# Optimization experiments

Measured on AMD Instinct MI355X. Metric: run time of the kernel, lower is better.

The kernel has to match this reference:

```python
import jax, jax.numpy as jnp
import numpy as np

B, M, N = 2, 256, 256
K, P, Q, D = 8, 512, 512, 64
R, Pp, Qp, Dp = 128, 512, 512, 64
TEMP = float(np.sqrt(Dp))  # softmax temperature = sqrt(D')


def _xavier(key, shape):
    # xavier_uniform over last two dims (fan_in, fan_out), matching torch init on (K, d, D)
    fan_in, fan_out = shape[-2], shape[-1]
    lim = float(np.sqrt(6.0 / (fan_in + fan_out)))
    return jax.random.uniform(key, shape, jnp.float32, -lim, lim)


def setup_inputs() -> dict:
    key = jax.random.key(0)
    ks = jax.random.split(key, 9)
    return {
        "z": jax.random.normal(ks[0], (B, M, N, R), jnp.float32),
        "y_q": jax.random.normal(ks[1], (B, N, Qp), jnp.float32),
        "x_k": jax.random.normal(ks[2], (B, M, Pp), jnp.float32),
        "Theta_x": _xavier(ks[3], (K, P, D)),
        "Theta_y": _xavier(ks[4], (K, Q, D)),
        "Lam_x": _xavier(ks[5], (K, Pp, Dp)),
        "Lam_y": _xavier(ks[6], (K, Qp, Dp)),
        "Lam_zx": _xavier(ks[7], (K, R, Dp)),
        "Lam_zy": _xavier(ks[8], (K, R, Dp)),
    }


def reference(z, y_q, x_k, Theta_x, Theta_y, Lam_x, Lam_y, Lam_zx, Lam_zy):
    # --- mixed attention scores ---
    xt = jnp.einsum('bmp,kpd->bkmd', x_k, Lam_x)          # [B,K,M,D']
    yt = jnp.einsum('bnq,kqd->bknd', y_q, Lam_y)          # [B,K,N,D']
    r = jnp.einsum('bkmd,bknd->bkmn', xt, yt)             # pairwise term
    zy = jnp.einsum('bmnr,krd->bkmnd', z, Lam_zy)         # [B,K,M,N,D'] (large)
    r = r + jnp.einsum('bkmnd,bkmd->bkmn', zy, xt)
    r = r + jnp.einsum('bknd,bmnr,krd->bkmn', yt, z, Lam_zx)
    # --- generalised convolution (mask=None, bias=False) ---
    a = jax.nn.softmax(r / TEMP, axis=-2)                 # softmax over M (column-wise)
    xv = jnp.einsum('bmp,kpd->bkmd', x_k, Theta_x)        # value projection
    y = jnp.einsum('bkmn,bkmd,kqd->bnq', a, xv, Theta_y)  # [B,N,Q]
    return y
```

## Files before the change

kernel.cpp:

```cpp
#include <hip/hip_runtime.h>
#include <hip/hip_bf16.h>

#define LOG2E_OVER_T 0.18033688011112042f

typedef __attribute__((ext_vector_type(8))) short short8;
typedef __attribute__((ext_vector_type(4))) float f32x4;
typedef unsigned short ushort_t;
typedef unsigned long long ull_t;

#define MFMA16(a, b, c) __builtin_amdgcn_mfma_f32_16x16x32_bf16(a, b, c, 0, 0, 0)

__device__ __forceinline__ ushort_t f2bf(float f) {
    union { float f; unsigned u; } v; v.f = f;
    unsigned r = (v.u + 0x7fffu + ((v.u >> 16) & 1u)) >> 16;
    return (ushort_t)r;
}

__device__ __forceinline__ void gload16(const float* g, float* l) {
    __builtin_amdgcn_global_load_lds(
        (const __attribute__((address_space(1))) void*)g,
        (__attribute__((address_space(3))) void*)l, 16, 0, 0);
}

__device__ __forceinline__ void split8(const float4 a, const float4 b,
                                       short8& hi, short8& lo)
{
    union { float f[8]; unsigned u[8]; } Z;
    Z.f[0] = a.x; Z.f[1] = a.y; Z.f[2] = a.z; Z.f[3] = a.w;
    Z.f[4] = b.x; Z.f[5] = b.y; Z.f[6] = b.z; Z.f[7] = b.w;
    union { unsigned u[4]; short8 s; } H, L;
    #pragma unroll
    for (int i = 0; i < 4; i++) {
        const unsigned u0 = Z.u[2 * i], u1 = Z.u[2 * i + 1];
        H.u[i] = __builtin_amdgcn_perm(u1, u0, 0x07060302u);
        union { unsigned u; float f; } h0, h1;
        h0.u = u0 & 0xffff0000u; h1.u = u1 & 0xffff0000u;
        union { float f; unsigned u; } l0, l1;
        l0.f = Z.f[2 * i] - h0.f; l1.f = Z.f[2 * i + 1] - h1.f;
        L.u[i] = __builtin_amdgcn_perm(l1.u, l0.u, 0x07060302u);
    }
    hi = H.s; lo = L.s;
}

__device__ __forceinline__ void mfma_core64(
    const ushort_t* __restrict__ Ag, int lda,
    const ushort_t* __restrict__ Btg, int ldb,
    int ksteps, f32x4 acc[2][2])
{
    __shared__ __align__(16) ushort_t As[64 * 40];
    __shared__ __align__(16) ushort_t Bs[64 * 40];
    const int t = threadIdx.x;
    const int srow = t >> 2, skc = (t & 3) * 8;
    const int lane = t & 63, w = t >> 6;
    const int wr = w >> 1, wc = w & 1;
    const int fr = lane & 15, kg = lane >> 4;
    const int aoff = (wr * 32 + fr) * 40 + kg * 8;
    const int boff = (wc * 32 + fr) * 40 + kg * 8;
    const long arow = (long)srow * lda + skc;
    const long brow = (long)srow * ldb + skc;

    short8 ra = *(const short8*)(Ag + arow);
    short8 rb = *(const short8*)(Btg + brow);
    for (int kt = 0; kt < ksteps; kt++) {
        __syncthreads();
        *(short8*)&As[srow * 40 + skc] = ra;
        *(short8*)&Bs[srow * 40 + skc] = rb;
        __syncthreads();
        if (kt + 1 < ksteps) {
            ra = *(const short8*)(Ag + arow + (kt + 1) * 32);
            rb = *(const short8*)(Btg + brow + (kt + 1) * 32);
        }
        short8 a0 = *(const short8*)&As[aoff];
        short8 a1 = *(const short8*)&As[aoff + 16 * 40];
        short8 b0 = *(const short8*)&Bs[boff];
        short8 b1 = *(const short8*)&Bs[boff + 16 * 40];
        acc[0][0] = MFMA16(a0, b0, acc[0][0]);
        acc[0][1] = MFMA16(a0, b1, acc[0][1]);
        acc[1][0] = MFMA16(a1, b0, acc[1][0]);
        acc[1][1] = MFMA16(a1, b1, acc[1][1]);
    }
}

__device__ __forceinline__ void zero_acc(f32x4 acc[2][2]) {
    const f32x4 z4 = {0.f, 0.f, 0.f, 0.f};
    acc[0][0] = z4; acc[0][1] = z4; acc[1][0] = z4; acc[1][1] = z4;
}

__global__ __launch_bounds__(256)
void convert_kernel(const float* __restrict__ x_k, const float* __restrict__ y_q,
                    const float* __restrict__ Lam_x, const float* __restrict__ Theta_x,
                    const float* __restrict__ Lam_y, const float* __restrict__ Lam_zy,
                    const float* __restrict__ Lam_zx, const float* __restrict__ Theta_y,
                    ushort_t* __restrict__ xkb, ushort_t* __restrict__ yqb,
                    ushort_t* __restrict__ WxTb, ushort_t* __restrict__ WyTb,
                    ushort_t* __restrict__ Zyb, ushort_t* __restrict__ Zxb,
                    ushort_t* __restrict__ TyTb, float* __restrict__ ssum)
{
    int i = blockIdx.x * 256 + threadIdx.x;
    if (i < 262144) { xkb[i] = f2bf(x_k[i]); return; }
    i -= 262144;
    if (i < 262144) { yqb[i] = f2bf(y_q[i]); return; }
    i -= 262144;
    if (i < 524288) {
        const int k = i >> 16, rem = i & 65535, dc = rem >> 9, p = i & 511;
        const float v = (dc < 64) ? Lam_x[((long)k * 512 + p) * 64 + dc]
                                  : Theta_x[((long)k * 512 + p) * 64 + dc - 64];
        WxTb[i] = f2bf(v); return;
    }
    i -= 524288;
    if (i < 262144) {
        const int k = i >> 15, d = (i >> 9) & 63, p = i & 511;
        WyTb[i] = f2bf(Lam_y[((long)k * 512 + p) * 64 + d]); return;
    }
    i -= 262144;
    if (i < 65536) { Zyb[i] = f2bf(Lam_zy[i]); return; }
    i -= 65536;
    if (i < 65536) { Zxb[i] = f2bf(Lam_zx[i]); return; }
    i -= 65536;
    if (i < 262144) {
        const int q = i >> 9, kd = i & 511, k = kd >> 6, d = kd & 63;
        TyTb[i] = f2bf(Theta_y[((long)k * 512 + q) * 64 + d]); return;
    }
    i -= 262144;
    ssum[i] = 0.f;
}

__global__ __launch_bounds__(256)
void proj_kernel(const ushort_t* __restrict__ xkb, const ushort_t* __restrict__ yqb,
                 const ushort_t* __restrict__ WxTb, const ushort_t* __restrict__ WyTb,
                 ushort_t* __restrict__ xtb, ushort_t* __restrict__ ytb,
                 ushort_t* __restrict__ xvTb)
{
    const int side = blockIdx.z;
    const int bx = blockIdx.x, by = blockIdx.y;
    if (side == 1 && bx >= 8) return;
    f32x4 acc[2][2]; zero_acc(acc);
    const int t = threadIdx.x, lane = t & 63, w = t >> 6;
    const int wr = w >> 1, wc = w & 1, fr = lane & 15, kg = lane >> 4;

    if (side == 0) {
        mfma_core64(xkb + (long)(by * 64) * 512, 512,
                    WxTb + (long)(bx * 64) * 512, 512, 16, acc);
        const int k = bx >> 1, isxv = bx & 1;
        #pragma unroll
        for (int mi = 0; mi < 2; mi++)
        #pragma unroll
        for (int ni = 0; ni < 2; ni++) {
            const int grow0 = by * 64 + wr * 32 + mi * 16 + kg * 4;
            const int b = grow0 >> 8, m0 = grow0 & 255;
            const int d = wc * 32 + ni * 16 + fr;
            if (!isxv) {
                #pragma unroll
                for (int j = 0; j < 4; j++)
                    xtb[(((long)(b * 8 + k)) * 256 + m0 + j) * 64 + d] = f2bf(acc[mi][ni][j]);
            } else {
                ull_t pk = (ull_t)f2bf(acc[mi][ni][0])
                         | ((ull_t)f2bf(acc[mi][ni][1]) << 16)
                         | ((ull_t)f2bf(acc[mi][ni][2]) << 32)
                         | ((ull_t)f2bf(acc[mi][ni][3]) << 48);
                *(ull_t*)&xvTb[(((long)(b * 8 + k)) * 64 + d) * 256 + m0] = pk;
            }
        }
    } else {
        mfma_core64(yqb + (long)(by * 64) * 512, 512,
                    WyTb + (long)(bx * 64) * 512, 512, 16, acc);
        const int k = bx;
        #pragma unroll
        for (int mi = 0; mi < 2; mi++)
        #pragma unroll
        for (int ni = 0; ni < 2; ni++)
        #pragma unroll
        for (int j = 0; j < 4; j++) {
            const int grow = by * 64 + wr * 32 + mi * 16 + kg * 4 + j;
            const int b = grow >> 8, n = grow & 255;
            const int d = wc * 32 + ni * 16 + fr;
            ytb[(((long)(b * 8 + k)) * 256 + n) * 64 + d] = f2bf(acc[mi][ni][j]);
        }
    }
}

__global__ __launch_bounds__(256)
void step2_kernel(const ushort_t* __restrict__ xtb, const ushort_t* __restrict__ ytb,
                  const ushort_t* __restrict__ Zyb, const ushort_t* __restrict__ Zxb,
                  ushort_t* __restrict__ wzyb, ushort_t* __restrict__ wzxb,
                  float* __restrict__ t1)
{
    const int bz = blockIdx.x;
    const int t = threadIdx.x, lane = t & 63, w = t >> 6;
    const int wr = w >> 1, wc = w & 1, fr = lane & 15, kg = lane >> 4;

    if (bz < 256) {
        const int which = bz >> 7, idx = bz & 127;
        const int bk = idx >> 3, tile = idx & 7, mt = tile >> 1, nt = tile & 1;
        const int k = bk & 7, b = bk >> 3;
        const ushort_t* Ag  = (which ? ytb : xtb) + ((long)bk * 256 + mt * 64) * 64;
        const ushort_t* Btg = (which ? Zxb : Zyb) + ((long)k * 128 + nt * 64) * 64;
        ushort_t* C = which ? wzxb : wzyb;
        f32x4 acc[2][2]; zero_acc(acc);
        mfma_core64(Ag, 64, Btg, 64, 2, acc);
        #pragma unroll
        for (int mi = 0; mi < 2; mi++)
        #pragma unroll
        for (int ni = 0; ni < 2; ni++)
        #pragma unroll
        for (int j = 0; j < 4; j++) {
            const int m_glob = mt * 64 + wr * 32 + mi * 16 + kg * 4 + j;
            const int r_glob = nt * 64 + wc * 32 + ni * 16 + fr;
            C[(((long)b * 256 + m_glob) * 8 + k) * 128 + r_glob] = f2bf(acc[mi][ni][j]);
        }
    } else {
        const int idx = bz - 256;
        const int bk = idx >> 4, tile = idx & 15, nt2 = tile >> 2, mt2 = tile & 3;
        f32x4 acc[2][2]; zero_acc(acc);
        mfma_core64(ytb + ((long)bk * 256 + nt2 * 64) * 64, 64,
                    xtb + ((long)bk * 256 + mt2 * 64) * 64, 64, 2, acc);
        #pragma unroll
        for (int mi = 0; mi < 2; mi++)
        #pragma unroll
        for (int ni = 0; ni < 2; ni++)
        #pragma unroll
        for (int j = 0; j < 4; j++) {
            const int n_glob = nt2 * 64 + wr * 32 + mi * 16 + kg * 4 + j;
            const int m_glob = mt2 * 64 + wc * 32 + ni * 16 + fr;
            t1[((long)bk * 256 + n_glob) * 256 + m_glob] = acc[mi][ni][j];
        }
    }
}

__global__ __launch_bounds__(256)
void fused_score(const float* __restrict__ z,
                 const ushort_t* __restrict__ wzyb, const ushort_t* __restrict__ wzxb,
                 const float* __restrict__ t1, ushort_t* __restrict__ Et,
                 float* __restrict__ ssum)
{
    const int nt = blockIdx.x, mt = blockIdx.y, b = blockIdx.z;
    const int nbase = nt * 16, m0 = mt * 8;
    __shared__ __align__(16) float zs[8192];
    __shared__ float sc[4][8][8][17];

    const int tid = threadIdx.x;
    const int lane = tid & 63, w = tid >> 6;
    const int fr = lane & 15, kg = lane >> 4;
    const int f8 = fr & 7;

    const int js   = w * 512 + lane;
    for (int c = 0; c < 2; c++) {
        const int n0c = nbase + c * 8;

        #pragma unroll
        for (int i = 0; i < 8; i++) {
            const int j   = js + i * 64;
            const int row = j >> 5;
            const int m_l = row >> 3, n_l = row & 7;
            const int sl  = (j & 31) ^ ((m_l ^ n_l) & 7);
            const float* src = z + (((long)b * 256 + m0 + m_l) * 256 + n0c + n_l) * 128 + sl * 4;
            gload16(src, &zs[(w * 8 + i) * 256]);
        }
        __syncthreads();

        #pragma unroll
        for (int m = 0; m < 8; m++) {
            const int row = m * 8 + f8;
            const int key = (m ^ f8) & 7;
            const int s0 = (w * 8 + kg * 2) ^ key, s1 = (w * 8 + kg * 2 + 1) ^ key;
            const float4 za = *(const float4*)&zs[row * 128 + s0 * 4];
            const float4 zb = *(const float4*)&zs[row * 128 + s1 * 4];
            const short8 wv = *(const short8*)(wzyb
                + (((long)b * 256 + m0 + m) * 8 + f8) * 128 + w * 32 + kg * 8);
            short8 hi, lo;
            split8(za, zb, hi, lo);
            f32x4 acc = {0.f, 0.f, 0.f, 0.f};
            acc = MFMA16(hi, wv, acc);
            acc = MFMA16(lo, wv, acc);
            if (fr < 8 && kg < 2) {
                #pragma unroll
                for (int j = 0; j < 4; j++)
                    sc[w][m][fr][c * 8 + kg * 4 + j] = acc[j];
            }
        }

        #pragma unroll
        for (int nl = 0; nl < 8; nl++) {
            const int row = f8 * 8 + nl;
            const int key = (f8 ^ nl) & 7;
            const int s0 = (w * 8 + kg * 2) ^ key, s1 = (w * 8 + kg * 2 + 1) ^ key;
            const float4 za = *(const float4*)&zs[row * 128 + s0 * 4];
            const float4 zb = *(const float4*)&zs[row * 128 + s1 * 4];
            const short8 wv = *(const short8*)(wzxb
                + (((long)b * 256 + n0c + nl) * 8 + f8) * 128 + w * 32 + kg * 8);
            short8 hi, lo;
            split8(za, zb, hi, lo);
            f32x4 acc = {0.f, 0.f, 0.f, 0.f};
            acc = MFMA16(hi, wv, acc);
            acc = MFMA16(lo, wv, acc);
            if (fr < 8 && kg < 2) {
                #pragma unroll
                for (int j = 0; j < 4; j++)
                    sc[w][kg * 4 + j][fr][c * 8 + nl] += acc[j];
            }
        }
        __syncthreads();
    }

    if (tid < 128) {
        const int k = tid >> 4, n = tid & 15;
        const float* tp = t1 + (((long)b * 8 + k) * 256 + nbase + n) * 256 + m0;
        const float4 t0 = *(const float4*)(tp);
        const float4 t4 = *(const float4*)(tp + 4);
        const float tv[8] = {t0.x, t0.y, t0.z, t0.w, t4.x, t4.y, t4.z, t4.w};
        float s8 = 0.f;
        ushort_t eb[8];
        #pragma unroll
        for (int m = 0; m < 8; m++) {
            const float s = sc[0][m][k][n] + sc[1][m][k][n]
                          + sc[2][m][k][n] + sc[3][m][k][n] + tv[m];
            const float e = exp2f(s * LOG2E_OVER_T);
            eb[m] = f2bf(e);
            s8 += e;
        }
        *(short8*)(Et + (((long)b * 8 + k) * 256 + nbase + n) * 256 + m0) = *(short8*)eb;
        atomicAdd(&ssum[(b * 8 + k) * 256 + nbase + n], s8);
    }
}

__global__ __launch_bounds__(256)
void ogemm_kernel(const ushort_t* __restrict__ Et, const ushort_t* __restrict__ xvTb,
                  const float* __restrict__ ssum, ushort_t* __restrict__ o2b)
{
    const int mt = blockIdx.x, bk = blockIdx.y;
    f32x4 acc[2][2]; zero_acc(acc);
    mfma_core64(Et + ((long)bk * 256 + mt * 64) * 256, 256,
                xvTb + (long)bk * 64 * 256, 256, 8, acc);
    const int t = threadIdx.x, lane = t & 63, w = t >> 6;
    const int wr = w >> 1, wc = w & 1, fr = lane & 15, kg = lane >> 4;
    const int b = bk >> 3, k = bk & 7;
    #pragma unroll
    for (int mi = 0; mi < 2; mi++)
    #pragma unroll
    for (int j = 0; j < 4; j++) {
        const int n = mt * 64 + wr * 32 + mi * 16 + kg * 4 + j;
        const float inv = 1.0f / ssum[bk * 256 + n];
        #pragma unroll
        for (int ni = 0; ni < 2; ni++) {
            const int d = wc * 32 + ni * 16 + fr;
            o2b[((long)b * 256 + n) * 512 + k * 64 + d] = f2bf(acc[mi][ni][j] * inv);
        }
    }
}

__global__ __launch_bounds__(256)
void ygemm_kernel(const ushort_t* __restrict__ o2b, const ushort_t* __restrict__ TyTb,
                  float* __restrict__ out)
{
    const int qt = blockIdx.x, mt = blockIdx.y, b = blockIdx.z;
    f32x4 acc[2][2]; zero_acc(acc);
    mfma_core64(o2b + ((long)b * 256 + mt * 64) * 512, 512,
                TyTb + (long)qt * 64 * 512, 512, 16, acc);
    const int t = threadIdx.x, lane = t & 63, w = t >> 6;
    const int wr = w >> 1, wc = w & 1, fr = lane & 15, kg = lane >> 4;
    #pragma unroll
    for (int mi = 0; mi < 2; mi++)
    #pragma unroll
    for (int ni = 0; ni < 2; ni++)
    #pragma unroll
    for (int j = 0; j < 4; j++) {
        const int n = mt * 64 + wr * 32 + mi * 16 + kg * 4 + j;
        const int q = qt * 64 + wc * 32 + ni * 16 + fr;
        out[((long)b * 256 + n) * 512 + q] = acc[mi][ni][j];
    }
}

extern "C" void kernel_launch(void* const* d_in, const int* in_sizes, int n_in,
                              void* d_out, int out_size, void* d_ws, size_t ws_size,
                              hipStream_t stream)
{
    const float* z       = (const float*)d_in[0];
    const float* y_q     = (const float*)d_in[1];
    const float* x_k     = (const float*)d_in[2];
    const float* Theta_x = (const float*)d_in[3];
    const float* Theta_y = (const float*)d_in[4];
    const float* Lam_x   = (const float*)d_in[5];
    const float* Lam_y   = (const float*)d_in[6];
    const float* Lam_zx  = (const float*)d_in[7];
    const float* Lam_zy  = (const float*)d_in[8];
    float* out = (float*)d_out;

    ushort_t* U = (ushort_t*)d_ws;
    ushort_t* xkb  = U;
    ushort_t* yqb  = U + 262144;
    ushort_t* WxTb = U + 524288;
    ushort_t* WyTb = U + 1048576;
    ushort_t* Zyb  = U + 1310720;
    ushort_t* Zxb  = U + 1376256;
    ushort_t* TyTb = U + 1441792;
    ushort_t* xtb  = U + 1703936;
    ushort_t* ytb  = U + 1966080;
    ushort_t* xvTb = U + 2228224;
    ushort_t* wzyb = U + 2490368;
    ushort_t* wzxb = U + 3014656;
    ushort_t* Et   = U + 3538944;
    ushort_t* o2b  = U + 4587520;
    float*    ssum = (float*)(U + 4849664);
    float*    t1   = (float*)(U + 4857856);

    convert_kernel<<<6672, 256, 0, stream>>>(x_k, y_q, Lam_x, Theta_x, Lam_y,
        Lam_zy, Lam_zx, Theta_y, xkb, yqb, WxTb, WyTb, Zyb, Zxb, TyTb, ssum);

    proj_kernel<<<dim3(16, 8, 2), 256, 0, stream>>>(xkb, yqb, WxTb, WyTb,
        xtb, ytb, xvTb);

    step2_kernel<<<512, 256, 0, stream>>>(xtb, ytb, Zyb, Zxb, wzyb, wzxb, t1);

    fused_score<<<dim3(16, 32, 2), 256, 0, stream>>>(z, wzyb, wzxb, t1,
        Et, ssum);

    ogemm_kernel<<<dim3(4, 16), 256, 0, stream>>>(Et, xvTb, ssum, o2b);

    ygemm_kernel<<<dim3(8, 4, 2), 256, 0, stream>>>(o2b, TyTb, out);
}
```

Before: 58.93 us.

## Prefetch both z chunks into doubled LDS and overlap second load with compute

The fused_score kernel now issues all async global-to-LDS loads for both n-chunks up front into a doubled shared buffer. It waits only on the first half with a partial vmcnt before computing chunk 0, so the second chunk's transfer overlaps that compute. The bf16 weight fragments are also preloaded into registers before the loop instead of being loaded inside it. This costs twice the LDS (64KB of z) and extra registers, which may reduce occupancy. The partial wait depends on the load issue order, and the padding on sc is removed.

```diff
diff --git a/kernel.cpp b/kernel.cpp
--- a/kernel.cpp
+++ b/kernel.cpp
@@ -235,72 +235,84 @@
 {
     const int nt = blockIdx.x, mt = blockIdx.y, b = blockIdx.z;
     const int nbase = nt * 16, m0 = mt * 8;
-    __shared__ __align__(16) float zs[8192];
-    __shared__ float sc[4][8][8][17];
+    __shared__ __align__(16) float zs[16384];
+    __shared__ float sc[4][8][8][16];
 
     const int tid = threadIdx.x;
     const int lane = tid & 63, w = tid >> 6;
     const int fr = lane & 15, kg = lane >> 4;
     const int f8 = fr & 7;
-
-    const int js   = w * 512 + lane;
-    for (int c = 0; c < 2; c++) {
-        const int n0c = nbase + c * 8;
-
-        #pragma unroll
-        for (int i = 0; i < 8; i++) {
-            const int j   = js + i * 64;
-            const int row = j >> 5;
-            const int m_l = row >> 3, n_l = row & 7;
-            const int sl  = (j & 31) ^ ((m_l ^ n_l) & 7);
-            const float* src = z + (((long)b * 256 + m0 + m_l) * 256 + n0c + n_l) * 128 + sl * 4;
-            gload16(src, &zs[(w * 8 + i) * 256]);
-        }
-        __syncthreads();
-
+    const int w8 = w * 8, kg2 = kg * 2;
+
+    short8 wy[8], wx[16];
+    #pragma unroll
+    for (int m = 0; m < 8; m++)
+        wy[m] = *(const short8*)(wzyb + (((long)b * 256 + m0 + m) * 8 + f8) * 128 + w * 32 + kg * 8);
+    #pragma unroll
+    for (int n = 0; n < 16; n++)
+        wx[n] = *(const short8*)(wzxb + (((long)b * 256 + nbase + n) * 8 + f8) * 128 + w * 32 + kg * 8);
+
+    #pragma unroll
+    for (int i = 0; i < 16; i++) {
+        const int ii = (i < 4) ? i : (i < 8 ? i + 4 : (i < 12 ? i - 4 : i));
+        const int j16 = w * 1024 + ii * 64 + lane;
+        const int row = j16 >> 5;
+        const int m_l = row >> 4, n_l = row & 15;
+        const int sl = (j16 & 31) ^ ((m_l ^ (n_l & 7)) & 7);
+        const float* src = z + (((long)b * 256 + m0 + m_l) * 256 + nbase + n_l) * 128 + sl * 4;
+        gload16(src, &zs[w * 4096 + ii * 256]);
+    }
+
+    auto compute_chunk = [&](const int c) {
         #pragma unroll
         for (int m = 0; m < 8; m++) {
-            const int row = m * 8 + f8;
+            const int row = m * 16 + c * 8 + f8;
             const int key = (m ^ f8) & 7;
-            const int s0 = (w * 8 + kg * 2) ^ key, s1 = (w * 8 + kg * 2 + 1) ^ key;
+            const int s0 = (w8 + kg2) ^ key, s1 = (w8 + kg2 + 1) ^ key;
             const float4 za = *(const float4*)&zs[row * 128 + s0 * 4];
             const float4 zb = *(const float4*)&zs[row * 128 + s1 * 4];
-            const short8 wv = *(const short8*)(wzyb
-                + (((long)b * 256 + m0 + m) * 8 + f8) * 128 + w * 32 + kg * 8);
             short8 hi, lo;
             split8(za, zb, hi, lo);
             f32x4 acc = {0.f, 0.f, 0.f, 0.f};
-            acc = MFMA16(hi, wv, acc);
-            acc = MFMA16(lo, wv, acc);
+            acc = MFMA16(hi, wy[m], acc);
+            acc = MFMA16(lo, wy[m], acc);
             if (fr < 8 && kg < 2) {
                 #pragma unroll
                 for (int j = 0; j < 4; j++)
                     sc[w][m][fr][c * 8 + kg * 4 + j] = acc[j];
             }
         }
-
         #pragma unroll
         for (int nl = 0; nl < 8; nl++) {
-            const int row = f8 * 8 + nl;
+            const int row = f8 * 16 + c * 8 + nl;
             const int key = (f8 ^ nl) & 7;
-            const int s0 = (w * 8 + kg * 2) ^ key, s1 = (w * 8 + kg * 2 + 1) ^ key;
+            const int s0 = (w8 + kg2) ^ key, s1 = (w8 + kg2 + 1) ^ key;
             const float4 za = *(const float4*)&zs[row * 128 + s0 * 4];
             const float4 zb = *(const float4*)&zs[row * 128 + s1 * 4];
-            const short8 wv = *(const short8*)(wzxb
-                + (((long)b * 256 + n0c + nl) * 8 + f8) * 128 + w * 32 + kg * 8);
             short8 hi, lo;
             split8(za, zb, hi, lo);
             f32x4 acc = {0.f, 0.f, 0.f, 0.f};
-            acc = MFMA16(hi, wv, acc);
-            acc = MFMA16(lo, wv, acc);
+            acc = MFMA16(hi, wx[c * 8 + nl], acc);
+            acc = MFMA16(lo, wx[c * 8 + nl], acc);
             if (fr < 8 && kg < 2) {
                 #pragma unroll
                 for (int j = 0; j < 4; j++)
                     sc[w][kg * 4 + j][fr][c * 8 + nl] += acc[j];
             }
         }
-        __syncthreads();
-    }
+    };
+
+    asm volatile("s_waitcnt vmcnt(8)" ::: "memory");
+    __builtin_amdgcn_s_barrier();
+    __builtin_amdgcn_sched_barrier(0);
+    compute_chunk(0);
+
+    asm volatile("s_waitcnt vmcnt(0)" ::: "memory");
+    __builtin_amdgcn_s_barrier();
+    __builtin_amdgcn_sched_barrier(0);
+    compute_chunk(1);
+
+    __syncthreads();
 
     if (tid < 128) {
         const int k = tid >> 4, n = tid & 15;
```

Result: slower. 62.74 us (+6.5%).

## Replace LDS-direct z loads with register staging and hoist weight loads

Applied to the files above, without the earlier changes.

Replaces the global_load_lds async copies of z with plain float4 global loads into registers, followed by swizzled LDS stores guarded by barriers. The Lam_zy weight fragments are hoisted out of the chunk loop and the Lam_zx fragments are loaded per chunk ahead of compute, so the inner MFMA loops no longer issue global loads. It also sets launch_bounds to 3 blocks per CU, drops the padding on the sc scratch array, and moves the trailing barrier out of the loop. This raises register pressure and adds a second barrier per chunk. Unpadded sc rows may cause LDS bank conflicts.

```diff
diff --git a/kernel.cpp b/kernel.cpp
--- a/kernel.cpp
+++ b/kernel.cpp
@@ -14,12 +14,6 @@
     union { float f; unsigned u; } v; v.f = f;
     unsigned r = (v.u + 0x7fffu + ((v.u >> 16) & 1u)) >> 16;
     return (ushort_t)r;
-}
-
-__device__ __forceinline__ void gload16(const float* g, float* l) {
-    __builtin_amdgcn_global_load_lds(
-        (const __attribute__((address_space(1))) void*)g,
-        (__attribute__((address_space(3))) void*)l, 16, 0, 0);
 }
 
 __device__ __forceinline__ void split8(const float4 a, const float4 b,
@@ -227,7 +221,7 @@
     }
 }
 
-__global__ __launch_bounds__(256)
+__global__ __launch_bounds__(256, 3)
 void fused_score(const float* __restrict__ z,
                  const ushort_t* __restrict__ wzyb, const ushort_t* __restrict__ wzxb,
                  const float* __restrict__ t1, ushort_t* __restrict__ Et,
@@ -236,42 +230,50 @@
     const int nt = blockIdx.x, mt = blockIdx.y, b = blockIdx.z;
     const int nbase = nt * 16, m0 = mt * 8;
     __shared__ __align__(16) float zs[8192];
-    __shared__ float sc[4][8][8][17];
+    __shared__ float sc[4][8][8][16];
 
     const int tid = threadIdx.x;
     const int lane = tid & 63, w = tid >> 6;
     const int fr = lane & 15, kg = lane >> 4;
     const int f8 = fr & 7;
-
-    const int js   = w * 512 + lane;
+    const int w8 = w * 8, kg2 = kg * 2;
+
+    short8 wy[8];
+    #pragma unroll
+    for (int m = 0; m < 8; m++)
+        wy[m] = *(const short8*)(wzyb + (((long)b * 256 + m0 + m) * 8 + f8) * 128 + w * 32 + kg * 8);
+
+    const int n_l = tid >> 5, sl_ = tid & 31;
+
     for (int c = 0; c < 2; c++) {
         const int n0c = nbase + c * 8;
 
-        #pragma unroll
-        for (int i = 0; i < 8; i++) {
-            const int j   = js + i * 64;
-            const int row = j >> 5;
-            const int m_l = row >> 3, n_l = row & 7;
-            const int sl  = (j & 31) ^ ((m_l ^ n_l) & 7);
-            const float* src = z + (((long)b * 256 + m0 + m_l) * 256 + n0c + n_l) * 128 + sl * 4;
-            gload16(src, &zs[(w * 8 + i) * 256]);
-        }
+        float4 zr[8];
+        #pragma unroll
+        for (int i = 0; i < 8; i++)
+            zr[i] = *(const float4*)(z + (((long)b * 256 + m0 + i) * 256 + n0c) * 128 + tid * 4);
+        short8 wxc[8];
+        #pragma unroll
+        for (int i = 0; i < 8; i++)
+            wxc[i] = *(const short8*)(wzxb + (((long)b * 256 + n0c + i) * 8 + f8) * 128 + w * 32 + kg * 8);
+
+        __syncthreads();
+        #pragma unroll
+        for (int i = 0; i < 8; i++)
+            *(float4*)&zs[((i * 8 + n_l) * 32 + (sl_ ^ ((i ^ n_l) & 7))) * 4] = zr[i];
         __syncthreads();
 
         #pragma unroll
         for (int m = 0; m < 8; m++) {
             const int row = m * 8 + f8;
             const int key = (m ^ f8) & 7;
-            const int s0 = (w * 8 + kg * 2) ^ key, s1 = (w * 8 + kg * 2 + 1) ^ key;
-            const float4 za = *(const float4*)&zs[row * 128 + s0 * 4];
-            const float4 zb = *(const float4*)&zs[row * 128 + s1 * 4];
-            const short8 wv = *(const short8*)(wzyb
-                + (((long)b * 256 + m0 + m) * 8 + f8) * 128 + w * 32 + kg * 8);
+            const float4 za = *(const float4*)&zs[(row * 32 + ((w8 + kg2) ^ key)) * 4];
+            const float4 zb = *(const float4*)&zs[(row * 32 + ((w8 + kg2 + 1) ^ key)) * 4];
             short8 hi, lo;
             split8(za, zb, hi, lo);
             f32x4 acc = {0.f, 0.f, 0.f, 0.f};
-            acc = MFMA16(hi, wv, acc);
-            acc = MFMA16(lo, wv, acc);
+            acc = MFMA16(hi, wy[m], acc);
+            acc = MFMA16(lo, wy[m], acc);
             if (fr < 8 && kg < 2) {
                 #pragma unroll
                 for (int j = 0; j < 4; j++)
@@ -283,24 +285,21 @@
         for (int nl = 0; nl < 8; nl++) {
             const int row = f8 * 8 + nl;
             const int key = (f8 ^ nl) & 7;
-            const int s0 = (w * 8 + kg * 2) ^ key, s1 = (w * 8 + kg * 2 + 1) ^ key;
-            const float4 za = *(const float4*)&zs[row * 128 + s0 * 4];
-            const float4 zb = *(const float4*)&zs[row * 128 + s1 * 4];
-            const short8 wv = *(const short8*)(wzxb
-                + (((long)b * 256 + n0c + nl) * 8 + f8) * 128 + w * 32 + kg * 8);
+            const float4 za = *(const float4*)&zs[(row * 32 + ((w8 + kg2) ^ key)) * 4];
+            const float4 zb = *(const float4*)&zs[(row * 32 + ((w8 + kg2 + 1) ^ key)) * 4];
             short8 hi, lo;
             split8(za, zb, hi, lo);
             f32x4 acc = {0.f, 0.f, 0.f, 0.f};
-            acc = MFMA16(hi, wv, acc);
-            acc = MFMA16(lo, wv, acc);
+            acc = MFMA16(hi, wxc[nl], acc);
+            acc = MFMA16(lo, wxc[nl], acc);
             if (fr < 8 && kg < 2) {
                 #pragma unroll
                 for (int j = 0; j < 4; j++)
                     sc[w][kg * 4 + j][fr][c * 8 + nl] += acc[j];
             }
         }
-        __syncthreads();
-    }
+    }
+    __syncthreads();
 
     if (tid < 128) {
         const int k = tid >> 4, n = tid & 15;
```

After: 72.24 us. 1.23x slower.

## Stage projected weights into LDS with swizzled layout in fused score kernel

Applied to the files above, without the earlier changes.

The producer kernel now writes the bf16 wzy/wzx projections in a per-8-row grouped, XOR-swizzled layout. The fused score kernel then bulk-loads each block's slice into shared memory with global_load_lds alongside the z tile, instead of issuing scattered per-lane global loads. This is meant to cut global load latency and uncoalesced traffic in the inner MFMA loops. The cost is 32KB of extra LDS per block, which may reduce occupancy. The sc padding was also removed, which may introduce bank conflicts.

```diff
diff --git a/kernel.cpp b/kernel.cpp
--- a/kernel.cpp
+++ b/kernel.cpp
@@ -16,7 +16,7 @@
     return (ushort_t)r;
 }
 
-__device__ __forceinline__ void gload16(const float* g, float* l) {
+__device__ __forceinline__ void gload16(const void* g, void* l) {
     __builtin_amdgcn_global_load_lds(
         (const __attribute__((address_space(1))) void*)g,
         (__attribute__((address_space(3))) void*)l, 16, 0, 0);
@@ -206,7 +206,10 @@
         for (int j = 0; j < 4; j++) {
             const int m_glob = mt * 64 + wr * 32 + mi * 16 + kg * 4 + j;
             const int r_glob = nt * 64 + wc * 32 + ni * 16 + fr;
-            C[(((long)b * 256 + m_glob) * 8 + k) * 128 + r_glob] = f2bf(acc[mi][ni][j]);
+            const int g = m_glob >> 3, lo = m_glob & 7;
+            const int ch = (r_glob >> 3) ^ (k & 7);
+            C[(((long)b * 32 + g) * 64 + lo * 8 + k) * 128 + ch * 8 + (r_glob & 7)]
+                = f2bf(acc[mi][ni][j]);
         }
     } else {
         const int idx = bz - 256;
@@ -235,26 +238,43 @@
 {
     const int nt = blockIdx.x, mt = blockIdx.y, b = blockIdx.z;
     const int nbase = nt * 16, m0 = mt * 8;
-    __shared__ __align__(16) float zs[8192];
-    __shared__ float sc[4][8][8][17];
+    __shared__ __align__(16) float    zs[8192];
+    __shared__ __align__(16) ushort_t wyl[8192];
+    __shared__ __align__(16) ushort_t wxl[8192];
+    __shared__ float sc[4][8][8][16];
 
     const int tid = threadIdx.x;
     const int lane = tid & 63, w = tid >> 6;
     const int fr = lane & 15, kg = lane >> 4;
     const int f8 = fr & 7;
-
-    const int js   = w * 512 + lane;
+    const int w8 = w * 8, kg2 = kg * 2;
+
+    #pragma unroll
+    for (int j = 0; j < 4; j++) {
+        const int c1k = w * 4 + j;
+        gload16(wzyb + (long)(b * 32 + mt) * 8192 + (c1k * 64 + lane) * 8,
+                &wyl[c1k * 512]);
+    }
+
+    const int js = w * 512 + lane;
+
     for (int c = 0; c < 2; c++) {
         const int n0c = nbase + c * 8;
 
         #pragma unroll
         for (int i = 0; i < 8; i++) {
-            const int j   = js + i * 64;
+            const int j = js + i * 64;
             const int row = j >> 5;
             const int m_l = row >> 3, n_l = row & 7;
-            const int sl  = (j & 31) ^ ((m_l ^ n_l) & 7);
-            const float* src = z + (((long)b * 256 + m0 + m_l) * 256 + n0c + n_l) * 128 + sl * 4;
-            gload16(src, &zs[(w * 8 + i) * 256]);
+            const int sl = (j & 31) ^ ((m_l ^ n_l) & 7);
+            gload16(z + (((long)b * 256 + m0 + m_l) * 256 + n0c + n_l) * 128 + sl * 4,
+                    &zs[(w * 8 + i) * 256]);
+        }
+        #pragma unroll
+        for (int j = 0; j < 4; j++) {
+            const int c1k = w * 4 + j;
+            gload16(wzxb + (long)(b * 32 + nt * 2 + c) * 8192 + (c1k * 64 + lane) * 8,
+                    &wxl[c1k * 512]);
         }
         __syncthreads();
 
@@ -262,11 +282,9 @@
         for (int m = 0; m < 8; m++) {
             const int row = m * 8 + f8;
             const int key = (m ^ f8) & 7;
-            const int s0 = (w * 8 + kg * 2) ^ key, s1 = (w * 8 + kg * 2 + 1) ^ key;
-            const float4 za = *(const float4*)&zs[row * 128 + s0 * 4];
-            const float4 zb = *(const float4*)&zs[row * 128 + s1 * 4];
-            const short8 wv = *(const short8*)(wzyb
-                + (((long)b * 256 + m0 + m) * 8 + f8) * 128 + w * 32 + kg * 8);
+            const float4 za = *(const float4*)&zs[row * 128 + (((w8 + kg2) ^ key)) * 4];
+            const float4 zb = *(const float4*)&zs[row * 128 + (((w8 + kg2 + 1) ^ key)) * 4];
+            const short8 wv = *(const short8*)&wyl[(m * 8 + f8) * 128 + (((w * 4 + kg) ^ f8)) * 8];
             short8 hi, lo;
             split8(za, zb, hi, lo);
             f32x4 acc = {0.f, 0.f, 0.f, 0.f};
@@ -283,11 +301,9 @@
         for (int nl = 0; nl < 8; nl++) {
             const int row = f8 * 8 + nl;
             const int key = (f8 ^ nl) & 7;
-            const int s0 = (w * 8 + kg * 2) ^ key, s1 = (w * 8 + kg * 2 + 1) ^ key;
-            const float4 za = *(const float4*)&zs[row * 128 + s0 * 4];
-            const float4 zb = *(const float4*)&zs[row * 128 + s1 * 4];
-            const short8 wv = *(const short8*)(wzxb
-                + (((long)b * 256 + n0c + nl) * 8 + f8) * 128 + w * 32 + kg * 8);
+            const float4 za = *(const float4*)&zs[row * 128 + (((w8 + kg2) ^ key)) * 4];
+            const float4 zb = *(const float4*)&zs[row * 128 + (((w8 + kg2 + 1) ^ key)) * 4];
+            const short8 wv = *(const short8*)&wxl[(nl * 8 + f8) * 128 + (((w * 4 + kg) ^ f8)) * 8];
             short8 hi, lo;
             split8(za, zb, hi, lo);
             f32x4 acc = {0.f, 0.f, 0.f, 0.f};
```

New measurement: 58.95 us. Within noise of the previous version (+0.0%).
